# Kernel tuning notes

Hardware: AMD Instinct MI355X
Metric: run time of the kernel (lower is better)

Reference implementation:

```python
import jax, jax.numpy as jnp
import numpy as np

TOP_K = 2

def setup_inputs() -> dict:
    key = jax.random.key(0)
    k1, k2 = jax.random.split(key)
    x = jax.random.normal(k1, (8192, 4096), dtype=jnp.float32)
    # nn.Linear(n_input, n_experts, bias=False): weight [n_experts, n_input]
    W = jax.random.normal(k2, (64, 4096), dtype=jnp.float32) * (1.0 / np.sqrt(4096))
    return {"x": x, "W": W}

def reference(x, W):
    logits = jnp.einsum('td,ed->te', x, W)            # [tokens, n_experts]
    probs = jax.nn.softmax(logits, axis=-1)
    top_w, top_i = jax.lax.top_k(probs, TOP_K)        # [tokens, k]
    rows = jnp.arange(probs.shape[0])[:, None]
    weights = jnp.zeros_like(probs).at[rows, top_i].set(top_w)
    return weights, top_i
```

## Files before the change

### kernel.cpp

```cpp
#include <hip/hip_runtime.h>
#include <math.h>


#define TOKENS 8192
#define DIM    4096
#define NEXP   64

#define KS     8
#define KSEG   (DIM / KS)
#define NCH    (KSEG / 32)

#define SBAR() __builtin_amdgcn_sched_barrier(0)

typedef __attribute__((ext_vector_type(8))) short  short8;
typedef __attribute__((ext_vector_type(4))) float  f32x4;
typedef __attribute__((ext_vector_type(8))) float  f32x8;

__device__ __forceinline__ void bf16split(float v, short& hi, short& lo) {
    unsigned u = __float_as_uint(v);
    hi = (short)(u >> 16);
    float r = v - __uint_as_float(u & 0xffff0000u);
    lo = (short)(__float_as_uint(r) >> 16);
}

__global__ __launch_bounds__(512, 2)
void tg_mfma(const float* __restrict__ x, const float* __restrict__ W,
             float* __restrict__ part) {
    __shared__ short8 Bls[2][NCH][4][64];

    const int tid  = threadIdx.x;
    const int lane = tid & 63;
    const int wave = tid >> 6;
    const int tg   = blockIdx.x >> 3;
    const int ks   = blockIdx.x & 7;
    const int t0   = tg * 128 + wave * 16;
    const int row  = lane & 15;
    const int grp  = lane >> 4;

#pragma unroll
    for (int s8 = 0; s8 < 8; ++s8) {
        const int s   = s8 * 512 + tid;
        const int c   = s >> 8;
        const int rem = s & 255;
        const int nt  = rem >> 6;
        const int ln  = rem & 63;
        const int e   = nt * 16 + (ln & 15);
        const int kb  = ks * KSEG + c * 32 + (ln >> 4) * 8;
        const f32x8 wv = *reinterpret_cast<const f32x8*>(W + (size_t)e * DIM + kb);
        short8 h, l;
#pragma unroll
        for (int j = 0; j < 8; ++j) {
            short hh, ll;
            bf16split(wv[j], hh, ll);
            h[j] = hh; l[j] = ll;
        }
        Bls[0][c][nt][ln] = h;
        Bls[1][c][nt][ln] = l;
    }
    __syncthreads();

    const float* xp = x + (size_t)(t0 + row) * DIM + ks * KSEG + grp * 8;

    f32x4 acc[4];
#pragma unroll
    for (int nt = 0; nt < 4; ++nt) acc[nt] = (f32x4){0.f, 0.f, 0.f, 0.f};

    short8 bA[8], bB[8];
    auto dsB = [&](short8 (&b)[8], int c) {
#pragma unroll
        for (int nt = 0; nt < 4; ++nt) {
            b[nt]     = Bls[0][c][nt][lane];
            b[4 + nt] = Bls[1][c][nt][lane];
        }
    };
    auto ldx = [&](int c) {
        return *reinterpret_cast<const f32x8*>(xp + c * 32);
    };
    auto cvt = [&](const f32x8& xv, short8& ah, short8& al) {
#pragma unroll
        for (int j = 0; j < 8; ++j) {
            short hh, ll;
            bf16split(xv[j], hh, ll);
            ah[j] = hh; al[j] = ll;
        }
    };
    auto mfma12 = [&](const short8& ah, const short8& al, const short8 (&b)[8]) {
        __builtin_amdgcn_s_setprio(1);
#pragma unroll
        for (int nt = 0; nt < 4; ++nt)
            acc[nt] = __builtin_amdgcn_mfma_f32_16x16x32_bf16(ah, b[nt], acc[nt], 0, 0, 0);
#pragma unroll
        for (int nt = 0; nt < 4; ++nt)
            acc[nt] = __builtin_amdgcn_mfma_f32_16x16x32_bf16(al, b[nt], acc[nt], 0, 0, 0);
#pragma unroll
        for (int nt = 0; nt < 4; ++nt)
            acc[nt] = __builtin_amdgcn_mfma_f32_16x16x32_bf16(ah, b[4 + nt], acc[nt], 0, 0, 0);
        __builtin_amdgcn_s_setprio(0);
    };

    f32x8 x0 = ldx(0), x1 = ldx(1), x2 = ldx(2),
          x3 = ldx(3), x4 = ldx(4), x5 = ldx(5);
    dsB(bA, 0);
    dsB(bB, 1);
    SBAR();

    short8 ah, al;
#define PPH(p, XA, XB)                                               \
    {                                                                \
        cvt(XA, ah, al);                                             \
        mfma12(ah, al, bA);                                          \
        cvt(XB, ah, al);                                             \
        mfma12(ah, al, bB);                                          \
        SBAR();                                                      \
        if (2*(p) + 2 < NCH) dsB(bA, 2*(p) + 2);                     \
        if (2*(p) + 3 < NCH) dsB(bB, 2*(p) + 3);                     \
        if (2*(p) + 6 < NCH) XA = ldx(2*(p) + 6);                    \
        if (2*(p) + 7 < NCH) XB = ldx(2*(p) + 7);                    \
        SBAR();                                                      \
    }

    PPH(0, x0, x1)
    PPH(1, x2, x3)
    PPH(2, x4, x5)
    PPH(3, x0, x1)
    PPH(4, x2, x3)
    PPH(5, x4, x5)
    PPH(6, x0, x1)
    PPH(7, x2, x3)
#undef PPH

    float* pp = part + ((size_t)ks * TOKENS + t0) * NEXP;
#pragma unroll
    for (int nt = 0; nt < 4; ++nt)
#pragma unroll
        for (int r = 0; r < 4; ++r)
            pp[(grp * 4 + r) * NEXP + nt * 16 + row] = acc[nt][r];
}

__global__ __launch_bounds__(256)
void tg_final(const float* __restrict__ part,
              float* __restrict__ out_w, float* __restrict__ out_i) {
    const int lane = threadIdx.x & 63;
    const int wv   = threadIdx.x >> 6;
    const int t    = blockIdx.x * 4 + wv;

    float s = 0.0f;
#pragma unroll
    for (int k = 0; k < KS; ++k)
        s += part[((size_t)k * TOKENS + t) * NEXP + lane];

    float m = s;
#pragma unroll
    for (int o = 32; o > 0; o >>= 1) m = fmaxf(m, __shfl_xor(m, o));
    float p = expf(s - m);
    float sum = p;
#pragma unroll
    for (int o = 32; o > 0; o >>= 1) sum += __shfl_xor(sum, o);
    const float prob = p / sum;

    float v1 = prob; int i1 = lane;
#pragma unroll
    for (int o = 32; o > 0; o >>= 1) {
        float ov = __shfl_xor(v1, o); int oi = __shfl_xor(i1, o);
        if (ov > v1 || (ov == v1 && oi < i1)) { v1 = ov; i1 = oi; }
    }
    float v2 = (lane == i1) ? -1.0f : prob; int i2 = lane;
#pragma unroll
    for (int o = 32; o > 0; o >>= 1) {
        float ov = __shfl_xor(v2, o); int oi = __shfl_xor(i2, o);
        if (ov > v2 || (ov == v2 && oi < i2)) { v2 = ov; i2 = oi; }
    }

    out_w[(size_t)t * NEXP + lane] = (lane == i1) ? v1 : (lane == i2) ? v2 : 0.0f;
    if (lane == 0) {
        out_i[(size_t)t * 2 + 0] = (float)i1;
        out_i[(size_t)t * 2 + 1] = (float)i2;
    }
}

extern "C" void kernel_launch(void* const* d_in, const int* in_sizes, int n_in,
                              void* d_out, int out_size, void* d_ws, size_t ws_size,
                              hipStream_t stream) {
    const float* x = (const float*)d_in[0];
    const float* W = (const float*)d_in[1];
    float* out_w = (float*)d_out;
    float* out_i = out_w + (size_t)TOKENS * NEXP;

    float* part = (float*)d_ws;

    tg_mfma <<<dim3((TOKENS / 128) * KS), dim3(512), 0, stream>>>(x, W, part);
    tg_final<<<dim3(TOKENS / 4), dim3(256), 0, stream>>>(part, out_w, out_i);
}
```

Baseline: 43.45 us.

## Stage W in two LDS halves and cut registers for 4-block occupancy

Halves the shared-memory buffer for the split-bf16 W tile, filling it in two stages of 256 K each with block barriers between them. It also drops the double-buffered B registers and reduces the x prefetch depth from six chunks to four. Together with launch_bounds raised to 4 blocks per CU, the aim is higher occupancy so more waves hide the latency of the x loads. The cost is an extra pair of __syncthreads plus a second W conversion pass mid-loop, and less software prefetching inside each wave.

Result: faster. 40.95 us (median of 3 runs) (-5.7%).

```diff
diff --git a/kernel.cpp b/kernel.cpp
--- a/kernel.cpp
+++ b/kernel.cpp
@@ -8,7 +8,9 @@
 
 #define KS     8
 #define KSEG   (DIM / KS)
-#define NCH    (KSEG / 32)
+#define NCHB   (KSEG / 32)
+#define PNK    256
+#define NCHP   (PNK / 32)
 
 #define SBAR() __builtin_amdgcn_sched_barrier(0)
 
@@ -23,10 +25,10 @@
     lo = (short)(__float_as_uint(r) >> 16);
 }
 
-__global__ __launch_bounds__(512, 2)
+__global__ __launch_bounds__(512, 4)
 void tg_mfma(const float* __restrict__ x, const float* __restrict__ W,
              float* __restrict__ part) {
-    __shared__ short8 Bls[2][NCH][4][64];
+    __shared__ short8 Bls[2][NCHP][4][64];
 
     const int tid  = threadIdx.x;
     const int lane = tid & 63;
@@ -37,44 +39,48 @@
     const int row  = lane & 15;
     const int grp  = lane >> 4;
 
+    const float* xp = x + (size_t)(t0 + row) * DIM + ks * KSEG + grp * 8;
+    auto ldx = [&](int c) {
+        return *reinterpret_cast<const f32x8*>(xp + c * 32);
+    };
+
+    f32x8 x0 = ldx(0), x1 = ldx(1), x2 = ldx(2), x3 = ldx(3);
+
+    auto prep = [&](int stage) {
+        const int k0 = ks * KSEG + stage * PNK;
 #pragma unroll
-    for (int s8 = 0; s8 < 8; ++s8) {
-        const int s   = s8 * 512 + tid;
-        const int c   = s >> 8;
-        const int rem = s & 255;
-        const int nt  = rem >> 6;
-        const int ln  = rem & 63;
-        const int e   = nt * 16 + (ln & 15);
-        const int kb  = ks * KSEG + c * 32 + (ln >> 4) * 8;
-        const f32x8 wv = *reinterpret_cast<const f32x8*>(W + (size_t)e * DIM + kb);
-        short8 h, l;
+        for (int s4 = 0; s4 < 4; ++s4) {
+            const int s   = s4 * 512 + tid;
+            const int c   = s >> 8;
+            const int rem = s & 255;
+            const int nt  = rem >> 6;
+            const int ln  = rem & 63;
+            const int e   = nt * 16 + (ln & 15);
+            const int kb  = k0 + c * 32 + (ln >> 4) * 8;
+            const f32x8 wv = *reinterpret_cast<const f32x8*>(W + (size_t)e * DIM + kb);
+            short8 h, l;
 #pragma unroll
-        for (int j = 0; j < 8; ++j) {
-            short hh, ll;
-            bf16split(wv[j], hh, ll);
-            h[j] = hh; l[j] = ll;
+            for (int j = 0; j < 8; ++j) {
+                short hh, ll;
+                bf16split(wv[j], hh, ll);
+                h[j] = hh; l[j] = ll;
+            }
+            Bls[0][c][nt][ln] = h;
+            Bls[1][c][nt][ln] = l;
         }
-        Bls[0][c][nt][ln] = h;
-        Bls[1][c][nt][ln] = l;
-    }
-    __syncthreads();
-
-    const float* xp = x + (size_t)(t0 + row) * DIM + ks * KSEG + grp * 8;
+    };
 
     f32x4 acc[4];
 #pragma unroll
     for (int nt = 0; nt < 4; ++nt) acc[nt] = (f32x4){0.f, 0.f, 0.f, 0.f};
 
-    short8 bA[8], bB[8];
-    auto dsB = [&](short8 (&b)[8], int c) {
+    short8 b[8];
+    auto dsB = [&](int c) {
 #pragma unroll
         for (int nt = 0; nt < 4; ++nt) {
             b[nt]     = Bls[0][c][nt][lane];
             b[4 + nt] = Bls[1][c][nt][lane];
         }
-    };
-    auto ldx = [&](int c) {
-        return *reinterpret_cast<const f32x8*>(xp + c * 32);
     };
     auto cvt = [&](const f32x8& xv, short8& ah, short8& al) {
 #pragma unroll
@@ -84,7 +90,7 @@
             ah[j] = hh; al[j] = ll;
         }
     };
-    auto mfma12 = [&](const short8& ah, const short8& al, const short8 (&b)[8]) {
+    auto mfma12 = [&](const short8& ah, const short8& al) {
         __builtin_amdgcn_s_setprio(1);
 #pragma unroll
         for (int nt = 0; nt < 4; ++nt)
@@ -98,36 +104,31 @@
         __builtin_amdgcn_s_setprio(0);
     };
 
-    f32x8 x0 = ldx(0), x1 = ldx(1), x2 = ldx(2),
-          x3 = ldx(3), x4 = ldx(4), x5 = ldx(5);
-    dsB(bA, 0);
-    dsB(bB, 1);
-    SBAR();
+    prep(0);
+    __syncthreads();
 
     short8 ah, al;
-#define PPH(p, XA, XB)                                               \
+#define PH(cg, cl, XV)                                               \
     {                                                                \
-        cvt(XA, ah, al);                                             \
-        mfma12(ah, al, bA);                                          \
-        cvt(XB, ah, al);                                             \
-        mfma12(ah, al, bB);                                          \
+        dsB(cl);                                                     \
         SBAR();                                                      \
-        if (2*(p) + 2 < NCH) dsB(bA, 2*(p) + 2);                     \
-        if (2*(p) + 3 < NCH) dsB(bB, 2*(p) + 3);                     \
-        if (2*(p) + 6 < NCH) XA = ldx(2*(p) + 6);                    \
-        if (2*(p) + 7 < NCH) XB = ldx(2*(p) + 7);                    \
+        cvt(XV, ah, al);                                             \
+        if ((cg) + 4 < NCHB) XV = ldx((cg) + 4);                     \
+        SBAR();                                                      \
+        mfma12(ah, al);                                              \
         SBAR();                                                      \
     }
 
-    PPH(0, x0, x1)
-    PPH(1, x2, x3)
-    PPH(2, x4, x5)
-    PPH(3, x0, x1)
-    PPH(4, x2, x3)
-    PPH(5, x4, x5)
-    PPH(6, x0, x1)
-    PPH(7, x2, x3)
-#undef PPH
+    PH(0, 0, x0)  PH(1, 1, x1)  PH(2, 2, x2)  PH(3, 3, x3)
+    PH(4, 4, x0)  PH(5, 5, x1)  PH(6, 6, x2)  PH(7, 7, x3)
+
+    __syncthreads();
+    prep(1);
+    __syncthreads();
+
+    PH(8,  0, x0)  PH(9,  1, x1)  PH(10, 2, x2)  PH(11, 3, x3)
+    PH(12, 4, x0)  PH(13, 5, x1)  PH(14, 6, x2)  PH(15, 7, x3)
+#undef PH
 
     float* pp = part + ((size_t)ks * TOKENS + t0) * NEXP;
 #pragma unroll
```
